# Kernel optimization log

Hardware: AMD Instinct MI355X
Metric: run time of the kernel (lower is better)

Reference implementation:

```python
import jax, jax.numpy as jnp
import numpy as np

E = 8            # num experts
D = 1024         # hidden size
F = 4096         # ffn hidden size
CAP_FACTOR = 2.0 # expert-choice capacity factor


def setup_inputs() -> dict:
    key = jax.random.key(0)
    ks = jax.random.split(key, 6)
    B, S = 8, 1024
    hidden_states = jax.random.normal(ks[0], (B, S, D), dtype=jnp.float32)
    Wg = jax.random.normal(ks[1], (D, E), dtype=jnp.float32) * (1.0 / np.sqrt(D))
    W1 = jax.random.normal(ks[2], (E, D, F), dtype=jnp.float32) * (1.0 / np.sqrt(D))
    b1 = jnp.zeros((E, F), dtype=jnp.float32)
    W2 = jax.random.normal(ks[3], (E, F, D), dtype=jnp.float32) * (1.0 / np.sqrt(F))
    b2 = jnp.zeros((E, D), dtype=jnp.float32)
    return {"hidden_states": hidden_states, "Wg": Wg, "W1": W1, "b1": b1,
            "W2": W2, "b2": b2}


def reference(hidden_states, Wg, W1, b1, W2, b2):
    B, S, d = hidden_states.shape
    T = B * S
    C = int(T * CAP_FACTOR / E)  # capacity per expert (static)

    x = hidden_states.reshape(T, d)                      # [T, D]
    gates = jax.nn.softmax(x @ Wg, axis=-1)              # [T, E] router probs

    # Expert-choice routing: each expert picks its top-C tokens.
    scores = gates.T                                     # [E, T]
    top_vals, idx = jax.lax.top_k(scores, C)             # [E, C]

    # Load-balancing aux loss (mean gate prob * fraction routed, per expert).
    frac_routed = jnp.zeros((T, E), gates.dtype).at[
        idx.reshape(-1), jnp.repeat(jnp.arange(E), C)].set(1.0).mean(axis=0)
    aux_loss = E * jnp.sum(gates.mean(axis=0) * frac_routed)

    # Grouped expert FFN on gathered tokens.
    xg = x[idx]                                          # [E, C, D]
    h = jax.nn.gelu(jnp.einsum('ecd,edf->ecf', xg, W1) + b1[:, None, :])
    yo = jnp.einsum('ecf,efd->ecd', h, W2) + b2[:, None, :]  # [E, C, D]

    # Weight by routing prob and scatter-add back to token positions.
    weighted = yo * top_vals[..., None]                  # [E, C, D]
    out = jnp.zeros((T, d), x.dtype).at[idx.reshape(-1)].add(
        weighted.reshape(-1, d))
    return out.reshape(B, S, d), aux_loss
```

## Files before the change

kernel.cpp:

```cpp
#include <hip/hip_runtime.h>
#include <hip/hip_bf16.h>

#define T_TOK 8192
#define E_EXP 8
#define D_HID 1024
#define F_FFN 4096
#define C_CAP 2048

typedef __attribute__((ext_vector_type(8))) short bf16x8;
typedef __attribute__((ext_vector_type(4))) float f32x4;

__device__ __forceinline__ void load_lds16(const void* g, void* l) {
    __builtin_amdgcn_global_load_lds(
        (const __attribute__((address_space(1))) unsigned int*)g,
        (__attribute__((address_space(3))) unsigned int*)l, 16, 0, 0);
}

__device__ __forceinline__ float gelu_fast(float v) {
    float z = v * (1.5957691216057308f + 0.07135481627f * v * v);
    return v / (1.0f + __expf(-z));
}

__global__ __launch_bounds__(256) void gating_kernel(
    const float* __restrict__ x, const float* __restrict__ Wg,
    float* __restrict__ gatesT, __hip_bfloat16* __restrict__ xbf,
    float* __restrict__ aux_out)
{
    const int token = blockIdx.x * 4 + (threadIdx.x >> 6);
    const int lane  = threadIdx.x & 63;
    if (token == 0 && lane == 0)
        aux_out[0] = (float)E_EXP * (float)C_CAP / (float)T_TOK;
    const float* xr = x + (size_t)token * D_HID;

    float acc[E_EXP];
#pragma unroll
    for (int e = 0; e < E_EXP; ++e) acc[e] = 0.0f;

#pragma unroll
    for (int it = 0; it < 4; ++it) {
        const int c4 = it * 64 + lane;
        float4 v = ((const float4*)xr)[c4];
        float vv[4] = {v.x, v.y, v.z, v.w};
        union { __hip_bfloat16 h[4]; short4 s; } u;
#pragma unroll
        for (int j = 0; j < 4; ++j) u.h[j] = __float2bfloat16(vv[j]);
        ((short4*)(xbf + (size_t)token * D_HID))[c4] = u.s;
        const float* wr0 = Wg + (size_t)c4 * 4 * E_EXP;
#pragma unroll
        for (int j = 0; j < 4; ++j)
#pragma unroll
            for (int e = 0; e < E_EXP; ++e) acc[e] += vv[j] * wr0[j * E_EXP + e];
    }
#pragma unroll
    for (int e = 0; e < E_EXP; ++e) {
        for (int off = 32; off; off >>= 1) acc[e] += __shfl_down(acc[e], off);
    }
    if (lane == 0) {
        float m = acc[0];
#pragma unroll
        for (int e = 1; e < E_EXP; ++e) m = fmaxf(m, acc[e]);
        float ex[E_EXP];
        float s = 0.0f;
#pragma unroll
        for (int e = 0; e < E_EXP; ++e) { ex[e] = expf(acc[e] - m); s += ex[e]; }
        float inv = 1.0f / s;
#pragma unroll
        for (int e = 0; e < E_EXP; ++e) gatesT[(size_t)e * T_TOK + token] = ex[e] * inv;
    }
}

__global__ __launch_bounds__(1024) void topk_kernel(
    const float* __restrict__ gatesT, int* __restrict__ topidx,
    float* __restrict__ topval, int* __restrict__ cnt, int* __restrict__ inv)
{
    __shared__ unsigned int hist[256];
    __shared__ unsigned int bc_v, bc_r;
    __shared__ unsigned int selcnt;

    const int e    = blockIdx.x;
    const int tid  = threadIdx.x;
    const int lane = tid & 63;
    const float* row = gatesT + (size_t)e * T_TOK;

    unsigned long long kreg[8];
#pragma unroll
    for (int p = 0; p < 8; ++p) {
        int i = tid + p * 1024;
        unsigned int b = __float_as_uint(row[i]);
        b = (b & 0x80000000u) ? ~b : (b | 0x80000000u);
        kreg[p] = ((unsigned long long)b << 32) | (unsigned int)(T_TOK - 1 - i);
    }
    if (tid == 0) selcnt = 0;

    unsigned long long prefix = 0ull, mask = 0ull;
    unsigned int rank = C_CAP;
    for (int byte = 7; byte >= 0; --byte) {
        if (tid < 256) hist[tid] = 0;
        __syncthreads();
        const int sh = byte * 8;
#pragma unroll
        for (int p = 0; p < 8; ++p) {
            unsigned long long k = kreg[p];
            if ((k & mask) == prefix)
                atomicAdd(&hist[(unsigned int)((k >> sh) & 255ull)], 1u);
        }
        __syncthreads();
        if (tid < 64) {
            unsigned int v0 = hist[tid * 4], v1 = hist[tid * 4 + 1];
            unsigned int v2 = hist[tid * 4 + 2], v3 = hist[tid * 4 + 3];
            unsigned int s3 = v3, s2 = v2 + s3, s1 = v1 + s2, s0 = v0 + s1;
            unsigned int t = s0;
#pragma unroll
            for (int off = 1; off < 64; off <<= 1) {
                unsigned int u = __shfl_down(t, off);
                if (lane + off < 64) t += u;
            }
            const unsigned int suf = t - s0;
            unsigned int ge[4] = {s0 + suf, s1 + suf, s2 + suf, s3 + suf};
            unsigned int gt[4] = {s1 + suf, s2 + suf, s3 + suf, suf};
#pragma unroll
            for (int j = 0; j < 4; ++j)
                if (ge[j] >= rank && gt[j] < rank) {
                    bc_v = (unsigned int)(tid * 4 + j); bc_r = rank - gt[j];
                }
        }
        __syncthreads();
        prefix |= ((unsigned long long)bc_v) << sh;
        mask   |= (0xFFull << sh);
        rank = bc_r;
        __syncthreads();
    }
    const unsigned long long thr = prefix;

#pragma unroll
    for (int p = 0; p < 8; ++p) {
        unsigned long long k = kreg[p];
        if (k >= thr) {
            int c = (int)atomicAdd(&selcnt, 1u);
            int idx = T_TOK - 1 - (int)(k & 0xFFFFFFFFull);
            unsigned int b = (unsigned int)(k >> 32);
            b = (b & 0x80000000u) ? (b & 0x7FFFFFFFu) : ~b;
            topidx[e * C_CAP + c] = idx;
            topval[e * C_CAP + c] = __uint_as_float(b);
            int slot = atomicAdd(&cnt[idx], 1);
            inv[idx * E_EXP + slot] = e * C_CAP + c;
        }
    }
}

__global__ __launch_bounds__(256) void transpose_bf16_kernel(
    const float* __restrict__ W1, __hip_bfloat16* __restrict__ W1t,
    const float* __restrict__ W2, __hip_bfloat16* __restrict__ W2t)
{
    __shared__ float tile[64][65];
    const int z = blockIdx.z;
    const float* in;
    __hip_bfloat16* out;
    int R, Cn, c0, r0;
    if (z < 8) {
        R = D_HID; Cn = F_FFN;
        in = W1 + (size_t)z * R * Cn; out = W1t + (size_t)z * R * Cn;
        c0 = blockIdx.x * 64; r0 = blockIdx.y * 64;
    } else {
        R = F_FFN; Cn = D_HID;
        in = W2 + (size_t)(z - 8) * R * Cn; out = W2t + (size_t)(z - 8) * R * Cn;
        c0 = blockIdx.y * 64; r0 = blockIdx.x * 64;
    }
    const int tid = threadIdx.x;

    const int lr = tid >> 4, lc4 = (tid & 15) * 4;
#pragma unroll
    for (int it = 0; it < 4; ++it) {
        int r = lr + it * 16;
        float4 v = *(const float4*)(in + (size_t)(r0 + r) * Cn + c0 + lc4);
        tile[r][lc4 + 0] = v.x; tile[r][lc4 + 1] = v.y;
        tile[r][lc4 + 2] = v.z; tile[r][lc4 + 3] = v.w;
    }
    __syncthreads();

    const int ocb = tid >> 3, j0 = (tid & 7) * 8;
#pragma unroll
    for (int it = 0; it < 2; ++it) {
        int oc = ocb + it * 32;
        union { __hip_bfloat16 h[8]; uint4 v; } u;
#pragma unroll
        for (int j = 0; j < 8; ++j) u.h[j] = __float2bfloat16(tile[j0 + j][oc]);
        *(uint4*)(out + (size_t)(c0 + oc) * R + r0 + j0) = u.v;
    }
}


#define BARS do { __builtin_amdgcn_s_barrier(); __builtin_amdgcn_sched_barrier(0); } while (0)
#define WLG  do { asm volatile("s_waitcnt lgkmcnt(0)" ::: "memory"); __builtin_amdgcn_sched_barrier(0); } while (0)
#define VMC8 asm volatile("s_waitcnt vmcnt(8)" ::: "memory")
#define VMC4 asm volatile("s_waitcnt vmcnt(4)" ::: "memory")
#define VMC0 asm volatile("s_waitcnt vmcnt(0)" ::: "memory")

#define STG_A3(hh, s, slot) do { int b_ = (slot) * 32768 + ((hh) << 14) + (w << 10); \
    load_lds16(Abase + (size_t)(aog[hh][0] + (s) * 128), smem + b_); \
    load_lds16(Abase + (size_t)(aog[hh][1] + (s) * 128), smem + b_ + 8192); } while (0)
#define STG_B3(hh, s) do { int b_ = 98304 + (((s) & 1) << 15) + ((hh) << 14) + (w << 10); \
    load_lds16(Bbase + (size_t)(bog[hh][0] + (s) * 128), smem + b_); \
    load_lds16(Bbase + (size_t)(bog[hh][1] + (s) * 128), smem + b_ + 8192); } while (0)

#define READ_A(mh) do { _Pragma("unroll") for (int mi = 0; mi < 4; ++mi) { \
    aF[mi][0] = *(const bf16x8*)(Ab + (arow + (mh) * 8192 + mi * 2048 + kc0)); \
    aF[mi][1] = *(const bf16x8*)(Ab + (arow + (mh) * 8192 + mi * 2048 + kc1)); } } while (0)
#define READ_B(nh, dst) do { _Pragma("unroll") for (int ni = 0; ni < 2; ++ni) { \
    dst[ni][0] = *(const bf16x8*)(Bb + (brow + (nh) * 4096 + ni * 2048 + kc0)); \
    dst[ni][1] = *(const bf16x8*)(Bb + (brow + (nh) * 4096 + ni * 2048 + kc1)); } } while (0)

#define QUAD(mh, nh, BF) do { \
    __builtin_amdgcn_s_setprio(1); \
    _Pragma("unroll") for (int mi = 0; mi < 4; ++mi) \
    _Pragma("unroll") for (int ni = 0; ni < 2; ++ni) { \
        acc[(mh)*4+mi][(nh)*2+ni] = __builtin_amdgcn_mfma_f32_16x16x32_bf16( \
            aF[mi][0], BF[ni][0], acc[(mh)*4+mi][(nh)*2+ni], 0, 0, 0); \
        acc[(mh)*4+mi][(nh)*2+ni] = __builtin_amdgcn_mfma_f32_16x16x32_bf16( \
            aF[mi][1], BF[ni][1], acc[(mh)*4+mi][(nh)*2+ni], 0, 0, 0); } \
    __builtin_amdgcn_s_setprio(0); } while (0)

#define GEMM_PROLOGUE_3B() do { \
    STG_A3(0, 0, 0); STG_A3(1, 0, 0); STG_A3(0, 1, 1); STG_A3(1, 1, 1); \
    STG_B3(0, 0); STG_B3(1, 0); STG_B3(0, 1); STG_B3(1, 1); \
    VMC4; BARS; } while (0)

#define GEMM_TILE_3B(t, NT) do { \
    const char* Ab = smem + ((t) % 3) * 32768; \
    const char* Bb = smem + 98304 + (((t) & 1) << 15); \
    const int sl2_ = ((t) + 2) % 3; \
     \
    READ_A(0); READ_B(0, bF0); \
    if ((t) + 2 < (NT)) STG_A3(0, (t) + 2, sl2_); \
    BARS; WLG; QUAD(0, 0, bF0); BARS; \
     \
    READ_B(1, bF1); \
    if ((t) + 2 < (NT)) STG_A3(1, (t) + 2, sl2_); \
    BARS; WLG; QUAD(0, 1, bF1); BARS; \
     \
    READ_A(1); \
    if ((t) + 2 < (NT)) STG_B3(0, (t) + 2); \
    BARS; WLG; QUAD(1, 1, bF1); BARS; \
     \
    if ((t) + 2 < (NT)) STG_B3(1, (t) + 2); \
    BARS; WLG; QUAD(1, 0, bF0); \
    if ((t) + 2 < (NT)) { VMC8; } else { VMC0; } \
    BARS; } while (0)

__global__ __launch_bounds__(512, 2) void gemm1_kernel(
    const __hip_bfloat16* __restrict__ xb,
    const __hip_bfloat16* __restrict__ W1t,
    const float* __restrict__ b1,
    const int* __restrict__ topidx,
    __hip_bfloat16* __restrict__ hbuf)
{
    __shared__ __align__(16) char smem[163840];
    const int tid = threadIdx.x;
    const int w = tid >> 6, lane = tid & 63;
    const int wr = w >> 2, wc = w & 3;
    const int fr = lane & 15, qlane = lane >> 4;

    const int bid = blockIdx.x;
    const int wg  = (bid & 7) * 128 + (bid >> 3);
    const int m0  = (wg & 7) * 256;
    const int n0  = ((wg >> 3) & 15) * 256;
    const int e   = wg >> 7;

    const char* Abase = (const char*)xb;
    const char* Bbase = (const char*)(W1t + (size_t)e * F_FFN * D_HID);

    const int cc = (tid & 7) ^ ((tid >> 3) & 7);
    int aog[2][2], bog[2][2];
#pragma unroll
    for (int hh = 0; hh < 2; ++hh)
#pragma unroll
        for (int j = 0; j < 2; ++j) {
            int r   = m0 + hh * 128 + j * 64 + (tid >> 3);
            int tok = topidx[e * C_CAP + r];
            aog[hh][j] = (tok * D_HID + cc * 8) * 2;
            int n = n0 + hh * 128 + j * 64 + (tid >> 3);
            bog[hh][j] = (n * D_HID + cc * 8) * 2;
        }

    const int arow = (wr * 128 + fr) * 128;
    const int brow = (wc * 64 + fr) * 128;
    const int kc0  = ((qlane)     ^ (lane & 7)) * 16;
    const int kc1  = ((4 + qlane) ^ (lane & 7)) * 16;

    bf16x8 aF[4][2], bF0[2][2], bF1[2][2];
    f32x4 acc[8][4];
#pragma unroll
    for (int mi = 0; mi < 8; ++mi)
#pragma unroll
        for (int ni = 0; ni < 4; ++ni) acc[mi][ni] = (f32x4){0.f, 0.f, 0.f, 0.f};

    GEMM_PROLOGUE_3B();
#pragma unroll 2
    for (int t = 0; t < 16; ++t) GEMM_TILE_3B(t, 16);

    const int q4 = qlane * 4;
    float b1v[4];
#pragma unroll
    for (int ni = 0; ni < 4; ++ni)
        b1v[ni] = b1[e * F_FFN + n0 + wc * 64 + ni * 16 + fr];
#pragma unroll
    for (int mi = 0; mi < 8; ++mi)
#pragma unroll
        for (int r = 0; r < 4; ++r) {
            const int row = wr * 128 + mi * 16 + q4 + r;
            char* rb = smem + row * 512;
            const int sw = (row & 7) << 4;
#pragma unroll
            for (int ni = 0; ni < 4; ++ni) {
                const int col2 = (wc * 64 + ni * 16 + fr) * 2;
                *(__hip_bfloat16*)(rb + (col2 ^ sw)) =
                    __float2bfloat16(gelu_fast(acc[mi][ni][r] + b1v[ni]));
            }
        }
    __syncthreads();
#pragma unroll
    for (int it = 0; it < 16; ++it) {
        const int row = it * 16 + w * 2 + (lane >> 5);
        const int cb  = (lane & 31) * 16;
        uint4 v = *(const uint4*)(smem + row * 512 + (cb ^ ((row & 7) << 4)));
        char* gp = (char*)(hbuf + ((size_t)e * C_CAP + m0 + row) * F_FFN + n0) + cb;
        *(uint4*)gp = v;
    }
}

__global__ __launch_bounds__(512, 2) void gemm2_kernel(
    const __hip_bfloat16* __restrict__ hbuf,
    const __hip_bfloat16* __restrict__ W2t,
    const float* __restrict__ b2,
    const float* __restrict__ topval,
    float* __restrict__ yo)
{
    __shared__ __align__(16) char smem[163840];
    const int tid = threadIdx.x;
    const int w = tid >> 6, lane = tid & 63;
    const int wr = w >> 2, wc = w & 3;
    const int fr = lane & 15, qlane = lane >> 4;

    const int bid = blockIdx.x;
    const int wg  = (bid & 7) * 32 + (bid >> 3);
    const int n0  = (wg & 3) * 256;
    const int m0  = ((wg >> 2) & 7) * 256;
    const int e   = wg >> 5;

    const char* Abase = (const char*)(hbuf + (size_t)e * C_CAP * F_FFN);
    const char* Bbase = (const char*)(W2t + (size_t)e * D_HID * F_FFN);

    const int cc = (tid & 7) ^ ((tid >> 3) & 7);
    int aog[2][2], bog[2][2];
#pragma unroll
    for (int hh = 0; hh < 2; ++hh)
#pragma unroll
        for (int j = 0; j < 2; ++j) {
            int r = m0 + hh * 128 + j * 64 + (tid >> 3);
            aog[hh][j] = (r * F_FFN + cc * 8) * 2;
            int n = n0 + hh * 128 + j * 64 + (tid >> 3);
            bog[hh][j] = (n * F_FFN + cc * 8) * 2;
        }

    const int arow = (wr * 128 + fr) * 128;
    const int brow = (wc * 64 + fr) * 128;
    const int kc0  = ((qlane)     ^ (lane & 7)) * 16;
    const int kc1  = ((4 + qlane) ^ (lane & 7)) * 16;

    bf16x8 aF[4][2], bF0[2][2], bF1[2][2];
    f32x4 acc[8][4];
#pragma unroll
    for (int mi = 0; mi < 8; ++mi)
#pragma unroll
        for (int ni = 0; ni < 4; ++ni) acc[mi][ni] = (f32x4){0.f, 0.f, 0.f, 0.f};

    GEMM_PROLOGUE_3B();
#pragma unroll 2
    for (int t = 0; t < 64; ++t) GEMM_TILE_3B(t, 64);

    const int q4 = qlane * 4;
    float b2v[4];
#pragma unroll
    for (int ni = 0; ni < 4; ++ni)
        b2v[ni] = b2[e * D_HID + n0 + wc * 64 + ni * 16 + fr];
#pragma unroll
    for (int mi = 0; mi < 8; ++mi) {
#pragma unroll
        for (int r = 0; r < 4; ++r) {
            const int row = m0 + wr * 128 + mi * 16 + q4 + r;
            const float g = topval[e * C_CAP + row];
            float* orow = yo + ((size_t)e * C_CAP + row) * D_HID + n0 + wc * 64;
#pragma unroll
            for (int ni = 0; ni < 4; ++ni)
                orow[ni * 16 + fr] = (acc[mi][ni][r] + b2v[ni]) * g;
        }
    }
}

__global__ __launch_bounds__(256) void combine_kernel(
    const float* __restrict__ yo, const int* __restrict__ cnt,
    const int* __restrict__ inv, float* __restrict__ out)
{
    const int t = blockIdx.x;
    const int n = cnt[t];
    const int c4 = threadIdx.x * 4;
    float4 a = {0.f, 0.f, 0.f, 0.f};
    for (int k = 0; k < n; ++k) {
        int ec = inv[t * E_EXP + k];
        float4 v = *(const float4*)(yo + (size_t)ec * D_HID + c4);
        a.x += v.x; a.y += v.y; a.z += v.z; a.w += v.w;
    }
    *(float4*)(out + (size_t)t * D_HID + c4) = a;
}

extern "C" void kernel_launch(void* const* d_in, const int* in_sizes, int n_in,
                              void* d_out, int out_size, void* d_ws, size_t ws_size,
                              hipStream_t stream) {
    const float* x  = (const float*)d_in[0];
    const float* Wg = (const float*)d_in[1];
    const float* W1 = (const float*)d_in[2];
    const float* b1 = (const float*)d_in[3];
    const float* W2 = (const float*)d_in[4];
    const float* b2 = (const float*)d_in[5];
    float* out = (float*)d_out;

    char* p = (char*)d_ws;
    float* gatesT = (float*)p;            p += (size_t)E_EXP * T_TOK * 4;
    int*   topidx = (int*)p;              p += (size_t)E_EXP * C_CAP * 4;
    float* topval = (float*)p;            p += (size_t)E_EXP * C_CAP * 4;
    int*   cnt    = (int*)p;              p += (size_t)T_TOK * 4;
    int*   inv    = (int*)p;              p += (size_t)T_TOK * E_EXP * 4;
    __hip_bfloat16* x_bf = (__hip_bfloat16*)p;  p += (size_t)T_TOK * D_HID * 2;
    __hip_bfloat16* W1t  = (__hip_bfloat16*)p;  p += (size_t)E_EXP * D_HID * F_FFN * 2;
    __hip_bfloat16* W2t  = (__hip_bfloat16*)p;  p += (size_t)E_EXP * D_HID * F_FFN * 2;
    __hip_bfloat16* hbuf = (__hip_bfloat16*)p;  p += (size_t)E_EXP * C_CAP * F_FFN * 2;
    float* yo = (float*)W1t;

    hipMemsetAsync(cnt, 0, (size_t)T_TOK * 4, stream);

    gating_kernel<<<T_TOK / 4, 256, 0, stream>>>(
        x, Wg, gatesT, x_bf, out + (size_t)T_TOK * D_HID);
    topk_kernel<<<E_EXP, 1024, 0, stream>>>(gatesT, topidx, topval, cnt, inv);

    {
        dim3 g(F_FFN / 64, D_HID / 64, 2 * E_EXP);
        transpose_bf16_kernel<<<g, 256, 0, stream>>>(W1, W1t, W2, W2t);
    }

    gemm1_kernel<<<1024, 512, 0, stream>>>(x_bf, W1t, b1, topidx, hbuf);
    gemm2_kernel<<<256, 512, 0, stream>>>(hbuf, W2t, b2, topval, yo);
    combine_kernel<<<T_TOK, 256, 0, stream>>>(yo, cnt, inv, out);
}
```

Before: 674.3 us.

## Retile gemm1 to 128x128 blocks and switch gemm2 to double-buffered LDS

gemm1 is rewritten to use 256-thread blocks with 128x128 output tiles (4096 blocks) and an 80KB LDS pipeline: A is triple-buffered, B double-buffered, and B is prefetched one K-step ahead. The aim is more blocks per CU and better load balance. gemm2 keeps its 256x256 tile but moves from a triple-buffered A scheme to double buffering for both A and B, cutting LDS from 160KB to 128KB, with its wait counts adjusted to match. Smaller gemm1 tiles reuse each loaded element less, and gemm2's shallower prefetch may expose more memory latency.

```diff
diff --git a/kernel.cpp b/kernel.cpp
--- a/kernel.cpp
+++ b/kernel.cpp
@@ -189,17 +189,147 @@
     }
 }
 
-
 #define BARS do { __builtin_amdgcn_s_barrier(); __builtin_amdgcn_sched_barrier(0); } while (0)
 #define WLG  do { asm volatile("s_waitcnt lgkmcnt(0)" ::: "memory"); __builtin_amdgcn_sched_barrier(0); } while (0)
-#define VMC8 asm volatile("s_waitcnt vmcnt(8)" ::: "memory")
 #define VMC4 asm volatile("s_waitcnt vmcnt(4)" ::: "memory")
 #define VMC0 asm volatile("s_waitcnt vmcnt(0)" ::: "memory")
 
-#define STG_A3(hh, s, slot) do { int b_ = (slot) * 32768 + ((hh) << 14) + (w << 10); \
+#define S1A(s, slot) do { _Pragma("unroll") for (int j = 0; j < 4; ++j) \
+    load_lds16(Abase + (size_t)(aog[j] + (s) * 128), smem + (slot) * 16384 + j * 4096 + w * 1024); } while (0)
+#define S1B(s) do { _Pragma("unroll") for (int j = 0; j < 4; ++j) \
+    load_lds16(Bbase + (size_t)(bog[j] + (s) * 128), smem + 49152 + ((s) & 1) * 16384 + j * 4096 + w * 1024); } while (0)
+
+__global__ __launch_bounds__(256, 2) void gemm1_kernel(
+    const __hip_bfloat16* __restrict__ xb,
+    const __hip_bfloat16* __restrict__ W1t,
+    const float* __restrict__ b1,
+    const int* __restrict__ topidx,
+    __hip_bfloat16* __restrict__ hbuf)
+{
+    __shared__ __align__(16) char smem[81920];
+    const int tid = threadIdx.x;
+    const int w = tid >> 6, lane = tid & 63;
+    const int wr = w >> 1, wc = w & 1;
+    const int fr = lane & 15, qlane = lane >> 4;
+
+    const int bid = blockIdx.x;
+    const int wg  = (bid & 7) * 512 + (bid >> 3);
+    const int e   = wg >> 9;
+    const int idx = wg & 511;
+    const int m0  = (idx & 15) * 128;
+    const int n0  = (idx >> 4) * 128;
+
+    const char* Abase = (const char*)xb;
+    const char* Bbase = (const char*)(W1t + (size_t)e * F_FFN * D_HID);
+
+    const int cc = (tid & 7) ^ ((tid >> 3) & 7);
+    int aog[4], bog[4];
+#pragma unroll
+    for (int j = 0; j < 4; ++j) {
+        int r   = j * 32 + (tid >> 3);
+        int tok = topidx[e * C_CAP + m0 + r];
+        aog[j] = (tok * D_HID + cc * 8) * 2;
+        int n = n0 + j * 32 + (tid >> 3);
+        bog[j] = (n * D_HID + cc * 8) * 2;
+    }
+
+    const int arow = (wr * 64 + fr) * 128;
+    const int brow = (wc * 64 + fr) * 128;
+    const int kc0  = ((qlane)     ^ (lane & 7)) * 16;
+    const int kc1  = ((4 + qlane) ^ (lane & 7)) * 16;
+
+    bf16x8 aF[4][2], bF[4][2];
+    f32x4 acc[4][4];
+#pragma unroll
+    for (int mi = 0; mi < 4; ++mi)
+#pragma unroll
+        for (int ni = 0; ni < 4; ++ni) acc[mi][ni] = (f32x4){0.f, 0.f, 0.f, 0.f};
+
+    S1A(0, 0); S1B(0); S1A(1, 1);
+    VMC4; BARS;
+
+    for (int t = 0; t < 16; ++t) {
+        const char* Ab = smem + (t % 3) * 16384;
+        const char* Bb = smem + 49152 + ((t & 1) << 14);
+#pragma unroll
+        for (int mi = 0; mi < 4; ++mi) {
+            aF[mi][0] = *(const bf16x8*)(Ab + (arow + mi * 2048 + kc0));
+            aF[mi][1] = *(const bf16x8*)(Ab + (arow + mi * 2048 + kc1));
+        }
+#pragma unroll
+        for (int ni = 0; ni < 2; ++ni) {
+            bF[ni][0] = *(const bf16x8*)(Bb + (brow + ni * 2048 + kc0));
+            bF[ni][1] = *(const bf16x8*)(Bb + (brow + ni * 2048 + kc1));
+        }
+        if (t + 1 < 16) S1B(t + 1);
+        WLG;
+        __builtin_amdgcn_s_setprio(1);
+#pragma unroll
+        for (int mi = 0; mi < 4; ++mi)
+#pragma unroll
+            for (int ni = 0; ni < 2; ++ni) {
+                acc[mi][ni] = __builtin_amdgcn_mfma_f32_16x16x32_bf16(
+                    aF[mi][0], bF[ni][0], acc[mi][ni], 0, 0, 0);
+                acc[mi][ni] = __builtin_amdgcn_mfma_f32_16x16x32_bf16(
+                    aF[mi][1], bF[ni][1], acc[mi][ni], 0, 0, 0);
+            }
+        __builtin_amdgcn_s_setprio(0);
+#pragma unroll
+        for (int ni = 2; ni < 4; ++ni) {
+            bF[ni][0] = *(const bf16x8*)(Bb + (brow + ni * 2048 + kc0));
+            bF[ni][1] = *(const bf16x8*)(Bb + (brow + ni * 2048 + kc1));
+        }
+        if (t + 2 < 16) { const int sl = (t + 2) % 3; S1A(t + 2, sl); }
+        WLG;
+        __builtin_amdgcn_s_setprio(1);
+#pragma unroll
+        for (int mi = 0; mi < 4; ++mi)
+#pragma unroll
+            for (int ni = 2; ni < 4; ++ni) {
+                acc[mi][ni] = __builtin_amdgcn_mfma_f32_16x16x32_bf16(
+                    aF[mi][0], bF[ni][0], acc[mi][ni], 0, 0, 0);
+                acc[mi][ni] = __builtin_amdgcn_mfma_f32_16x16x32_bf16(
+                    aF[mi][1], bF[ni][1], acc[mi][ni], 0, 0, 0);
+            }
+        __builtin_amdgcn_s_setprio(0);
+        if (t + 2 < 16) { VMC4; } else { VMC0; }
+        BARS;
+    }
+
+    const int q4 = qlane * 4;
+    float b1v[4];
+#pragma unroll
+    for (int ni = 0; ni < 4; ++ni)
+        b1v[ni] = b1[e * F_FFN + n0 + wc * 64 + ni * 16 + fr];
+#pragma unroll
+    for (int mi = 0; mi < 4; ++mi)
+#pragma unroll
+        for (int r = 0; r < 4; ++r) {
+            const int row = wr * 64 + mi * 16 + q4 + r;
+            char* rb = smem + row * 256;
+            const int sw = (row & 7) << 4;
+#pragma unroll
+            for (int ni = 0; ni < 4; ++ni) {
+                const int col2 = (wc * 64 + ni * 16 + fr) * 2;
+                *(__hip_bfloat16*)(rb + (col2 ^ sw)) =
+                    __float2bfloat16(gelu_fast(acc[mi][ni][r] + b1v[ni]));
+            }
+        }
+    __syncthreads();
+#pragma unroll
+    for (int it = 0; it < 8; ++it) {
+        const int row = it * 16 + (tid >> 4);
+        const int cb  = (tid & 15) * 16;
+        uint4 v = *(const uint4*)(smem + row * 256 + (cb ^ ((row & 7) << 4)));
+        char* gp = (char*)(hbuf + ((size_t)e * C_CAP + m0 + row) * F_FFN + n0) + cb;
+        *(uint4*)gp = v;
+    }
+}
+
+#define STG2_A(hh, s) do { int b_ = (((s) & 1) << 15) + ((hh) << 14) + (w << 10); \
     load_lds16(Abase + (size_t)(aog[hh][0] + (s) * 128), smem + b_); \
     load_lds16(Abase + (size_t)(aog[hh][1] + (s) * 128), smem + b_ + 8192); } while (0)
-#define STG_B3(hh, s) do { int b_ = 98304 + (((s) & 1) << 15) + ((hh) << 14) + (w << 10); \
+#define STG2_B(hh, s) do { int b_ = 65536 + (((s) & 1) << 15) + ((hh) << 14) + (w << 10); \
     load_lds16(Bbase + (size_t)(bog[hh][0] + (s) * 128), smem + b_); \
     load_lds16(Bbase + (size_t)(bog[hh][1] + (s) * 128), smem + b_ + 8192); } while (0)
 
@@ -220,113 +350,27 @@
             aF[mi][1], BF[ni][1], acc[(mh)*4+mi][(nh)*2+ni], 0, 0, 0); } \
     __builtin_amdgcn_s_setprio(0); } while (0)
 
-#define GEMM_PROLOGUE_3B() do { \
-    STG_A3(0, 0, 0); STG_A3(1, 0, 0); STG_A3(0, 1, 1); STG_A3(1, 1, 1); \
-    STG_B3(0, 0); STG_B3(1, 0); STG_B3(0, 1); STG_B3(1, 1); \
+#define GEMM_PROLOGUE_G() do { \
+    STG2_A(0, 0); STG2_A(1, 0); STG2_B(0, 0); STG2_B(1, 0); \
+    STG2_B(0, 1); STG2_B(1, 1); \
     VMC4; BARS; } while (0)
 
-#define GEMM_TILE_3B(t, NT) do { \
-    const char* Ab = smem + ((t) % 3) * 32768; \
-    const char* Bb = smem + 98304 + (((t) & 1) << 15); \
-    const int sl2_ = ((t) + 2) % 3; \
-     \
+#define GEMM_TILE_G(t, NT) do { \
+    const char* Ab = smem + (((t) & 1) << 15); \
+    const char* Bb = smem + 65536 + (((t) & 1) << 15); \
     READ_A(0); READ_B(0, bF0); \
-    if ((t) + 2 < (NT)) STG_A3(0, (t) + 2, sl2_); \
+    if ((t) + 1 < (NT)) STG2_A(0, (t) + 1); \
     BARS; WLG; QUAD(0, 0, bF0); BARS; \
-     \
     READ_B(1, bF1); \
-    if ((t) + 2 < (NT)) STG_A3(1, (t) + 2, sl2_); \
+    if ((t) + 1 < (NT)) STG2_A(1, (t) + 1); \
     BARS; WLG; QUAD(0, 1, bF1); BARS; \
-     \
     READ_A(1); \
-    if ((t) + 2 < (NT)) STG_B3(0, (t) + 2); \
+    if ((t) + 2 < (NT)) STG2_B(0, (t) + 2); \
     BARS; WLG; QUAD(1, 1, bF1); BARS; \
-     \
-    if ((t) + 2 < (NT)) STG_B3(1, (t) + 2); \
+    if ((t) + 2 < (NT)) STG2_B(1, (t) + 2); \
     BARS; WLG; QUAD(1, 0, bF0); \
-    if ((t) + 2 < (NT)) { VMC8; } else { VMC0; } \
+    if ((t) + 2 < (NT)) { VMC4; } else { VMC0; } \
     BARS; } while (0)
-
-__global__ __launch_bounds__(512, 2) void gemm1_kernel(
-    const __hip_bfloat16* __restrict__ xb,
-    const __hip_bfloat16* __restrict__ W1t,
-    const float* __restrict__ b1,
-    const int* __restrict__ topidx,
-    __hip_bfloat16* __restrict__ hbuf)
-{
-    __shared__ __align__(16) char smem[163840];
-    const int tid = threadIdx.x;
-    const int w = tid >> 6, lane = tid & 63;
-    const int wr = w >> 2, wc = w & 3;
-    const int fr = lane & 15, qlane = lane >> 4;
-
-    const int bid = blockIdx.x;
-    const int wg  = (bid & 7) * 128 + (bid >> 3);
-    const int m0  = (wg & 7) * 256;
-    const int n0  = ((wg >> 3) & 15) * 256;
-    const int e   = wg >> 7;
-
-    const char* Abase = (const char*)xb;
-    const char* Bbase = (const char*)(W1t + (size_t)e * F_FFN * D_HID);
-
-    const int cc = (tid & 7) ^ ((tid >> 3) & 7);
-    int aog[2][2], bog[2][2];
-#pragma unroll
-    for (int hh = 0; hh < 2; ++hh)
-#pragma unroll
-        for (int j = 0; j < 2; ++j) {
-            int r   = m0 + hh * 128 + j * 64 + (tid >> 3);
-            int tok = topidx[e * C_CAP + r];
-            aog[hh][j] = (tok * D_HID + cc * 8) * 2;
-            int n = n0 + hh * 128 + j * 64 + (tid >> 3);
-            bog[hh][j] = (n * D_HID + cc * 8) * 2;
-        }
-
-    const int arow = (wr * 128 + fr) * 128;
-    const int brow = (wc * 64 + fr) * 128;
-    const int kc0  = ((qlane)     ^ (lane & 7)) * 16;
-    const int kc1  = ((4 + qlane) ^ (lane & 7)) * 16;
-
-    bf16x8 aF[4][2], bF0[2][2], bF1[2][2];
-    f32x4 acc[8][4];
-#pragma unroll
-    for (int mi = 0; mi < 8; ++mi)
-#pragma unroll
-        for (int ni = 0; ni < 4; ++ni) acc[mi][ni] = (f32x4){0.f, 0.f, 0.f, 0.f};
-
-    GEMM_PROLOGUE_3B();
-#pragma unroll 2
-    for (int t = 0; t < 16; ++t) GEMM_TILE_3B(t, 16);
-
-    const int q4 = qlane * 4;
-    float b1v[4];
-#pragma unroll
-    for (int ni = 0; ni < 4; ++ni)
-        b1v[ni] = b1[e * F_FFN + n0 + wc * 64 + ni * 16 + fr];
-#pragma unroll
-    for (int mi = 0; mi < 8; ++mi)
-#pragma unroll
-        for (int r = 0; r < 4; ++r) {
-            const int row = wr * 128 + mi * 16 + q4 + r;
-            char* rb = smem + row * 512;
-            const int sw = (row & 7) << 4;
-#pragma unroll
-            for (int ni = 0; ni < 4; ++ni) {
-                const int col2 = (wc * 64 + ni * 16 + fr) * 2;
-                *(__hip_bfloat16*)(rb + (col2 ^ sw)) =
-                    __float2bfloat16(gelu_fast(acc[mi][ni][r] + b1v[ni]));
-            }
-        }
-    __syncthreads();
-#pragma unroll
-    for (int it = 0; it < 16; ++it) {
-        const int row = it * 16 + w * 2 + (lane >> 5);
-        const int cb  = (lane & 31) * 16;
-        uint4 v = *(const uint4*)(smem + row * 512 + (cb ^ ((row & 7) << 4)));
-        char* gp = (char*)(hbuf + ((size_t)e * C_CAP + m0 + row) * F_FFN + n0) + cb;
-        *(uint4*)gp = v;
-    }
-}
 
 __global__ __launch_bounds__(512, 2) void gemm2_kernel(
     const __hip_bfloat16* __restrict__ hbuf,
@@ -335,7 +379,7 @@
     const float* __restrict__ topval,
     float* __restrict__ yo)
 {
-    __shared__ __align__(16) char smem[163840];
+    __shared__ __align__(16) char smem[131072];
     const int tid = threadIdx.x;
     const int w = tid >> 6, lane = tid & 63;
     const int wr = w >> 2, wc = w & 3;
@@ -374,9 +418,9 @@
 #pragma unroll
         for (int ni = 0; ni < 4; ++ni) acc[mi][ni] = (f32x4){0.f, 0.f, 0.f, 0.f};
 
-    GEMM_PROLOGUE_3B();
+    GEMM_PROLOGUE_G();
 #pragma unroll 2
-    for (int t = 0; t < 64; ++t) GEMM_TILE_3B(t, 64);
+    for (int t = 0; t < 64; ++t) GEMM_TILE_G(t, 64);
 
     const int q4 = qlane * 4;
     float b2v[4];
@@ -447,7 +491,7 @@
         transpose_bf16_kernel<<<g, 256, 0, stream>>>(W1, W1t, W2, W2t);
     }
 
-    gemm1_kernel<<<1024, 512, 0, stream>>>(x_bf, W1t, b1, topidx, hbuf);
+    gemm1_kernel<<<4096, 256, 0, stream>>>(x_bf, W1t, b1, topidx, hbuf);
     gemm2_kernel<<<256, 512, 0, stream>>>(hbuf, W2t, b2, topval, yo);
     combine_kernel<<<T_TOK, 256, 0, stream>>>(yo, cnt, inv, out);
 }
```

Measured after the change: 686.6 us. About the same (+1.8%).

## Revert A operand to double-buffered LDS pipeline with one-tile prefetch

Applied to the files above, without the earlier changes.

The A operand goes back from a triple-buffered LDS ring prefetching two tiles ahead to a double buffer prefetching one tile ahead, while B stays two-deep. This cuts LDS per block from 160KB to 128KB. It also drops the sched_barrier fences around barriers and waits, and removes the unroll-2 pragma on the k-loop. In exchange, A global loads have less time to hide latency, and the compiler is freer to reorder instructions around the barriers.

```diff
diff --git a/kernel.cpp b/kernel.cpp
--- a/kernel.cpp
+++ b/kernel.cpp
@@ -190,16 +190,15 @@
 }
 
 
-#define BARS do { __builtin_amdgcn_s_barrier(); __builtin_amdgcn_sched_barrier(0); } while (0)
-#define WLG  do { asm volatile("s_waitcnt lgkmcnt(0)" ::: "memory"); __builtin_amdgcn_sched_barrier(0); } while (0)
-#define VMC8 asm volatile("s_waitcnt vmcnt(8)" ::: "memory")
+#define BARS __builtin_amdgcn_s_barrier()
+#define WLG  asm volatile("s_waitcnt lgkmcnt(0)" ::: "memory")
 #define VMC4 asm volatile("s_waitcnt vmcnt(4)" ::: "memory")
 #define VMC0 asm volatile("s_waitcnt vmcnt(0)" ::: "memory")
 
-#define STG_A3(hh, s, slot) do { int b_ = (slot) * 32768 + ((hh) << 14) + (w << 10); \
+#define G_STAGE_A(hh, s) do { int b_ = (((s) & 1) << 15) + ((hh) << 14) + (w << 10); \
     load_lds16(Abase + (size_t)(aog[hh][0] + (s) * 128), smem + b_); \
     load_lds16(Abase + (size_t)(aog[hh][1] + (s) * 128), smem + b_ + 8192); } while (0)
-#define STG_B3(hh, s) do { int b_ = 98304 + (((s) & 1) << 15) + ((hh) << 14) + (w << 10); \
+#define G_STAGE_B(hh, s) do { int b_ = 65536 + (((s) & 1) << 15) + ((hh) << 14) + (w << 10); \
     load_lds16(Bbase + (size_t)(bog[hh][0] + (s) * 128), smem + b_); \
     load_lds16(Bbase + (size_t)(bog[hh][1] + (s) * 128), smem + b_ + 8192); } while (0)
 
@@ -220,31 +219,30 @@
             aF[mi][1], BF[ni][1], acc[(mh)*4+mi][(nh)*2+ni], 0, 0, 0); } \
     __builtin_amdgcn_s_setprio(0); } while (0)
 
-#define GEMM_PROLOGUE_3B() do { \
-    STG_A3(0, 0, 0); STG_A3(1, 0, 0); STG_A3(0, 1, 1); STG_A3(1, 1, 1); \
-    STG_B3(0, 0); STG_B3(1, 0); STG_B3(0, 1); STG_B3(1, 1); \
+#define GEMM_PROLOGUE() do { \
+    G_STAGE_A(0, 0); G_STAGE_A(1, 0); G_STAGE_B(0, 0); G_STAGE_B(1, 0); \
+    G_STAGE_B(0, 1); G_STAGE_B(1, 1); \
     VMC4; BARS; } while (0)
 
-#define GEMM_TILE_3B(t, NT) do { \
-    const char* Ab = smem + ((t) % 3) * 32768; \
-    const char* Bb = smem + 98304 + (((t) & 1) << 15); \
-    const int sl2_ = ((t) + 2) % 3; \
+#define GEMM_TILE(t, NT) do { \
+    const char* Ab = smem + (((t) & 1) << 15); \
+    const char* Bb = smem + 65536 + (((t) & 1) << 15); \
      \
     READ_A(0); READ_B(0, bF0); \
-    if ((t) + 2 < (NT)) STG_A3(0, (t) + 2, sl2_); \
+    if ((t) + 1 < (NT)) G_STAGE_A(0, (t) + 1); \
     BARS; WLG; QUAD(0, 0, bF0); BARS; \
      \
     READ_B(1, bF1); \
-    if ((t) + 2 < (NT)) STG_A3(1, (t) + 2, sl2_); \
+    if ((t) + 1 < (NT)) G_STAGE_A(1, (t) + 1); \
     BARS; WLG; QUAD(0, 1, bF1); BARS; \
      \
     READ_A(1); \
-    if ((t) + 2 < (NT)) STG_B3(0, (t) + 2); \
+    if ((t) + 2 < (NT)) G_STAGE_B(0, (t) + 2); \
     BARS; WLG; QUAD(1, 1, bF1); BARS; \
      \
-    if ((t) + 2 < (NT)) STG_B3(1, (t) + 2); \
+    if ((t) + 2 < (NT)) G_STAGE_B(1, (t) + 2); \
     BARS; WLG; QUAD(1, 0, bF0); \
-    if ((t) + 2 < (NT)) { VMC8; } else { VMC0; } \
+    if ((t) + 2 < (NT)) { VMC4; } else { VMC0; } \
     BARS; } while (0)
 
 __global__ __launch_bounds__(512, 2) void gemm1_kernel(
@@ -254,7 +252,7 @@
     const int* __restrict__ topidx,
     __hip_bfloat16* __restrict__ hbuf)
 {
-    __shared__ __align__(16) char smem[163840];
+    __shared__ __align__(16) char smem[131072];
     const int tid = threadIdx.x;
     const int w = tid >> 6, lane = tid & 63;
     const int wr = w >> 2, wc = w & 3;
@@ -294,9 +292,8 @@
 #pragma unroll
         for (int ni = 0; ni < 4; ++ni) acc[mi][ni] = (f32x4){0.f, 0.f, 0.f, 0.f};
 
-    GEMM_PROLOGUE_3B();
-#pragma unroll 2
-    for (int t = 0; t < 16; ++t) GEMM_TILE_3B(t, 16);
+    GEMM_PROLOGUE();
+    for (int t = 0; t < 16; ++t) GEMM_TILE(t, 16);
 
     const int q4 = qlane * 4;
     float b1v[4];
@@ -335,7 +332,7 @@
     const float* __restrict__ topval,
     float* __restrict__ yo)
 {
-    __shared__ __align__(16) char smem[163840];
+    __shared__ __align__(16) char smem[131072];
     const int tid = threadIdx.x;
     const int w = tid >> 6, lane = tid & 63;
     const int wr = w >> 2, wc = w & 3;
@@ -374,9 +371,8 @@
 #pragma unroll
         for (int ni = 0; ni < 4; ++ni) acc[mi][ni] = (f32x4){0.f, 0.f, 0.f, 0.f};
 
-    GEMM_PROLOGUE_3B();
-#pragma unroll 2
-    for (int t = 0; t < 64; ++t) GEMM_TILE_3B(t, 64);
+    GEMM_PROLOGUE();
+    for (int t = 0; t < 64; ++t) GEMM_TILE(t, 64);
 
     const int q4 = qlane * 4;
     float b2v[4];
```

Measured after the change: 665.1 us. No clear change (-1.4%).
